# Performance work log

Hardware: AMD Instinct MI355X
Metric: run time of the kernel (lower is better)

## Reference

```python
import jax, jax.numpy as jnp
from jax import lax
import numpy as np

I, H, O = 4, 64, 4  # input_size, hidden_size, fc out


def setup_inputs() -> dict:
    key = jax.random.key(0)
    ks = jax.random.split(key, 7)
    B, T = 2048, 512
    s_ih = 1.0 / np.sqrt(H)  # PyTorch default init scale
    x = jax.random.normal(ks[0], (B, T, I), dtype=jnp.float32)
    W_ih = jax.random.uniform(ks[1], (4 * H, I), minval=-s_ih, maxval=s_ih, dtype=jnp.float32)
    W_hh = jax.random.uniform(ks[2], (4 * H, H), minval=-s_ih, maxval=s_ih, dtype=jnp.float32)
    b_ih = jax.random.uniform(ks[3], (4 * H,), minval=-s_ih, maxval=s_ih, dtype=jnp.float32)
    b_hh = jax.random.uniform(ks[4], (4 * H,), minval=-s_ih, maxval=s_ih, dtype=jnp.float32)
    W_fc = jax.random.uniform(ks[5], (O, H), minval=-s_ih, maxval=s_ih, dtype=jnp.float32)
    b_fc = jax.random.uniform(ks[6], (O,), minval=-s_ih, maxval=s_ih, dtype=jnp.float32)
    return {"x": x, "W_ih": W_ih, "W_hh": W_hh, "b_ih": b_ih, "b_hh": b_hh,
            "W_fc": W_fc, "b_fc": b_fc}


def reference(x, W_ih, W_hh, b_ih, b_hh, W_fc, b_fc):
    B = x.shape[0]
    # Precompute input contribution to all gates for every timestep: [B, T, 4H]
    xg = jnp.einsum('bti,gi->btg', x, W_ih) + (b_ih + b_hh)

    def step(carry, xt):
        h, c = carry                      # [B, H], [B, H]
        gates = xt + h @ W_hh.T           # [B, 4H]; PyTorch gate order i,f,g,o
        i, f, g, o = jnp.split(gates, 4, axis=-1)
        c = jax.nn.sigmoid(f) * c + jax.nn.sigmoid(i) * jnp.tanh(g)
        h = jax.nn.sigmoid(o) * jnp.tanh(c)
        return (h, c), None

    h0 = jnp.zeros((B, H), dtype=x.dtype)
    (h, c), _ = lax.scan(step, (h0, h0), jnp.swapaxes(xg, 0, 1))  # scan over T
    hidden = h[None]                      # [1, B, H] (num_layers*dirs = 1)
    return hidden @ W_fc.T + b_fc         # [1, B, O]
```

## Files before the change

kernel.cpp:

```cpp
#include <hip/hip_runtime.h>

typedef _Float16 half8 __attribute__((ext_vector_type(8)));
typedef _Float16 half4 __attribute__((ext_vector_type(4)));
typedef float f32x4 __attribute__((ext_vector_type(4)));

#define TT 512
#define HH 64
#define MB 8
#define S  72
#define XS 2056

__device__ __forceinline__ float xor8(float v) {
    return __builtin_bit_cast(float,
        __builtin_amdgcn_update_dpp(0, __builtin_bit_cast(int, v),
                                    0x128 ,
                                    0xF, 0xF, true));
}

__global__ __launch_bounds__(512, 1)
void lstm_v12(const float* __restrict__ x,
              const float* __restrict__ W_ih,
              const float* __restrict__ W_hh,
              const float* __restrict__ b_ih,
              const float* __restrict__ b_hh,
              const float* __restrict__ W_fc,
              const float* __restrict__ b_fc,
              float* __restrict__ out)
{
    __shared__ __align__(16) _Float16 st[2][8 * S];
    __shared__ __align__(16) _Float16 xbuf[MB * XS];

    const int tid = threadIdx.x;
    const int w   = tid >> 6;
    const int l   = tid & 63;
    const int q   = l >> 4;
    const int col = l & 15;
    const int b0  = blockIdx.x * MB;
    const int xcol = col & 7;
    const bool lo = (col < 8);

    const float kN = -1.4426950408889634f;
    const float kP =  2.8853900817779268f;

    half8 aw[2][3];
    #pragma unroll
    for (int p = 0; p < 2; ++p) {
        const int r = 64 * (col & 3) + 8 * w + 2 * (col >> 2) + p;
        const float scale = ((col & 3) == 2) ? kP : kN;
        #pragma unroll
        for (int c = 0; c < 2; ++c) {
            const float* src = W_hh + r * HH + 32 * c + 8 * q;
            half8 v;
            #pragma unroll
            for (int j = 0; j < 8; ++j) v[j] = (_Float16)(src[j] * scale);
            aw[p][c] = v;
        }
        half8 v = {};
        if (q == 0) {
            #pragma unroll
            for (int j = 0; j < 4; ++j) v[j] = (_Float16)(W_ih[r * 4 + j] * scale);
            v[4] = (_Float16)((b_ih[r] + b_hh[r]) * scale);
        }
        aw[p][2] = v;
    }

    #pragma unroll
    for (int it = 0; it < (MB * TT) / 512; ++it) {
        const int task = tid + it * 512;
        const int b = task >> 9, t = task & 511;
        float4 v = *(const float4*)(x + ((size_t)(b0 + b) * TT + t) * 4);
        half4 hx;
        hx[0] = (_Float16)v.x; hx[1] = (_Float16)v.y;
        hx[2] = (_Float16)v.z; hx[3] = (_Float16)v.w;
        *(half4*)&xbuf[b * XS + t * 4] = hx;
    }

    {
        _Float16* p0 = &st[0][0];
        for (int i = tid; i < 2 * 8 * S; i += 512) p0[i] = (_Float16)0.f;
    }
    __syncthreads();

    float cs = 0.f;
    const int wrow = xcol * S + 8 * w + 2 * q + (col >> 3);
    const _Float16 hone = (_Float16)1.0f, hzer = (_Float16)0.f;
    const f32x4 z4 = {0.f, 0.f, 0.f, 0.f};

    f32x4 accx0, accx1;
    {
        half4 xv = *(const half4*)&xbuf[xcol * XS + 0];
        half8 bx = {xv[0], xv[1], xv[2], xv[3], hone, hzer, hzer, hzer};
        accx0 = __builtin_amdgcn_mfma_f32_16x16x32_f16(aw[0][2], bx, z4, 0, 0, 0);
        accx1 = __builtin_amdgcn_mfma_f32_16x16x32_f16(aw[1][2], bx, z4, 0, 0, 0);
    }

    #pragma unroll 4
    for (int t = 0; t < TT; ++t) {
        const int rb = t & 1, wb = rb ^ 1;
        const _Float16* sr = &st[rb][0];

        half8 bh0 = *(const half8*)&sr[xcol * S +      8 * q];
        half8 bh1 = *(const half8*)&sr[xcol * S + 32 + 8 * q];
        half4 xv2 = *(const half4*)&xbuf[xcol * XS + (t + 1) * 4];

        f32x4 a0 = __builtin_amdgcn_mfma_f32_16x16x32_f16(aw[0][0], bh0, accx0, 0, 0, 0);
        f32x4 a1 = __builtin_amdgcn_mfma_f32_16x16x32_f16(aw[1][0], bh0, accx1, 0, 0, 0);
        a0 = __builtin_amdgcn_mfma_f32_16x16x32_f16(aw[0][1], bh1, a0, 0, 0, 0);
        a1 = __builtin_amdgcn_mfma_f32_16x16x32_f16(aw[1][1], bh1, a1, 0, 0, 0);

        {
            half8 bx2 = {xv2[0], xv2[1], xv2[2], xv2[3], hone, hzer, hzer, hzer};
            accx0 = __builtin_amdgcn_mfma_f32_16x16x32_f16(aw[0][2], bx2, z4, 0, 0, 0);
            accx1 = __builtin_amdgcn_mfma_f32_16x16x32_f16(aw[1][2], bx2, z4, 0, 0, 0);
        }

        const float s0 = xor8(a1[0]);
        const float s1 = xor8(a1[1]);
        const float s2 = xor8(a1[2]);
        const float s3 = xor8(a1[3]);
        const float gi = lo ? a0[0] : s0;
        const float gf = lo ? a0[1] : s1;
        const float gg = lo ? a0[2] : s2;
        const float go = lo ? a0[3] : s3;

        const float EI = __builtin_amdgcn_exp2f(gi);
        const float EF = __builtin_amdgcn_exp2f(gf);
        const float EG = __builtin_amdgcn_exp2f(gg);
        const float rF = __builtin_amdgcn_rcpf(1.f + EF);
        const float r1 = __builtin_amdgcn_rcpf((1.f + EI) * (EG + 1.f));
        cs = cs * rF + (EG - 1.f) * r1;
        const float EO = __builtin_amdgcn_exp2f(go);
        const float EC = __builtin_amdgcn_exp2f(kP * cs);
        const float r2 = __builtin_amdgcn_rcpf((1.f + EO) * (EC + 1.f));
        const float hn = (EC - 1.f) * r2;

        st[wb][wrow] = (_Float16)hn;
        __syncthreads();
    }

    if (tid < MB * 4) {
        const int b = tid >> 2, o = tid & 3;
        float s = b_fc[o];
        const float* wf = W_fc + o * HH;
        #pragma unroll
        for (int k = 0; k < HH; ++k)
            s = fmaf((float)st[0][b * S + k], wf[k], s);
        out[(size_t)(b0 + b) * 4 + o] = s;
    }
}

extern "C" void kernel_launch(void* const* d_in, const int* in_sizes, int n_in,
                              void* d_out, int out_size, void* d_ws, size_t ws_size,
                              hipStream_t stream) {
    const float* x    = (const float*)d_in[0];
    const float* W_ih = (const float*)d_in[1];
    const float* W_hh = (const float*)d_in[2];
    const float* b_ih = (const float*)d_in[3];
    const float* b_hh = (const float*)d_in[4];
    const float* W_fc = (const float*)d_in[5];
    const float* b_fc = (const float*)d_in[6];
    float* out = (float*)d_out;
    lstm_v12<<<2048 / MB, 512, 0, stream>>>(x, W_ih, W_hh, b_ih, b_hh, W_fc, b_fc, out);
}
```

Measured before the change: 229.0 us.

## Shrink LSTM blocks to 4 batch rows with 4 waves and 2 blocks per CU

Each block now handles 4 batch sequences with 256 threads (4 waves), and each wave computes 16 hidden units through 4 MFMA tiles instead of 2. This removes the DPP cross-lane shuffle, since each lane picks its gate values from the right tile with selects. Launch bounds now allow 2 blocks per CU and the grid doubles to 512 blocks. The aim is cheaper per-step barriers across fewer waves and more blocks to overlap each other's serial time steps. In exchange each wave issues twice the MFMAs per step, and 3 of every 4 tile columns are wasted because only 4 batch columns are live.

```diff
diff --git a/kernel.cpp b/kernel.cpp
--- a/kernel.cpp
+++ b/kernel.cpp
@@ -6,19 +6,12 @@
 
 #define TT 512
 #define HH 64
-#define MB 8
-#define S  72
+#define MB 4
+#define S  88
 #define XS 2056
 
-__device__ __forceinline__ float xor8(float v) {
-    return __builtin_bit_cast(float,
-        __builtin_amdgcn_update_dpp(0, __builtin_bit_cast(int, v),
-                                    0x128 ,
-                                    0xF, 0xF, true));
-}
-
-__global__ __launch_bounds__(512, 1)
-void lstm_v12(const float* __restrict__ x,
+__global__ __launch_bounds__(256, 2)
+void lstm_v13(const float* __restrict__ x,
               const float* __restrict__ W_ih,
               const float* __restrict__ W_hh,
               const float* __restrict__ b_ih,
@@ -27,7 +20,7 @@
               const float* __restrict__ b_fc,
               float* __restrict__ out)
 {
-    __shared__ __align__(16) _Float16 st[2][8 * S];
+    __shared__ __align__(16) _Float16 st[2][MB * S];
     __shared__ __align__(16) _Float16 xbuf[MB * XS];
 
     const int tid = threadIdx.x;
@@ -35,17 +28,17 @@
     const int l   = tid & 63;
     const int q   = l >> 4;
     const int col = l & 15;
+    const int bt  = col & 3;
+    const int g   = col >> 2;
     const int b0  = blockIdx.x * MB;
-    const int xcol = col & 7;
-    const bool lo = (col < 8);
 
     const float kN = -1.4426950408889634f;
     const float kP =  2.8853900817779268f;
 
-    half8 aw[2][3];
+    half8 aw[4][3];
     #pragma unroll
-    for (int p = 0; p < 2; ++p) {
-        const int r = 64 * (col & 3) + 8 * w + 2 * (col >> 2) + p;
+    for (int p = 0; p < 4; ++p) {
+        const int r = 64 * (col & 3) + 16 * w + 4 * p + (col >> 2);
         const float scale = ((col & 3) == 2) ? kP : kN;
         #pragma unroll
         for (int c = 0; c < 2; ++c) {
@@ -65,8 +58,8 @@
     }
 
     #pragma unroll
-    for (int it = 0; it < (MB * TT) / 512; ++it) {
-        const int task = tid + it * 512;
+    for (int it = 0; it < (MB * TT) / 256; ++it) {
+        const int task = tid + it * 256;
         const int b = task >> 9, t = task & 511;
         float4 v = *(const float4*)(x + ((size_t)(b0 + b) * TT + t) * 4);
         half4 hx;
@@ -75,23 +68,23 @@
         *(half4*)&xbuf[b * XS + t * 4] = hx;
     }
 
-    {
-        _Float16* p0 = &st[0][0];
-        for (int i = tid; i < 2 * 8 * S; i += 512) p0[i] = (_Float16)0.f;
-    }
+    for (int i = tid; i < 2 * MB * S; i += 256) (&st[0][0])[i] = (_Float16)0.f;
     __syncthreads();
 
     float cs = 0.f;
-    const int wrow = xcol * S + 8 * w + 2 * q + (col >> 3);
+    const int wrow = bt * S + 16 * w + 4 * g + q;
     const _Float16 hone = (_Float16)1.0f, hzer = (_Float16)0.f;
     const f32x4 z4 = {0.f, 0.f, 0.f, 0.f};
+    const bool s1 = (g & 1) != 0, s2 = (g & 2) != 0;
 
-    f32x4 accx0, accx1;
+    f32x4 accx0, accx1, accx2, accx3;
     {
-        half4 xv = *(const half4*)&xbuf[xcol * XS + 0];
+        half4 xv = *(const half4*)&xbuf[bt * XS + 0];
         half8 bx = {xv[0], xv[1], xv[2], xv[3], hone, hzer, hzer, hzer};
         accx0 = __builtin_amdgcn_mfma_f32_16x16x32_f16(aw[0][2], bx, z4, 0, 0, 0);
         accx1 = __builtin_amdgcn_mfma_f32_16x16x32_f16(aw[1][2], bx, z4, 0, 0, 0);
+        accx2 = __builtin_amdgcn_mfma_f32_16x16x32_f16(aw[2][2], bx, z4, 0, 0, 0);
+        accx3 = __builtin_amdgcn_mfma_f32_16x16x32_f16(aw[3][2], bx, z4, 0, 0, 0);
     }
 
     #pragma unroll 4
@@ -99,29 +92,33 @@
         const int rb = t & 1, wb = rb ^ 1;
         const _Float16* sr = &st[rb][0];
 
-        half8 bh0 = *(const half8*)&sr[xcol * S +      8 * q];
-        half8 bh1 = *(const half8*)&sr[xcol * S + 32 + 8 * q];
-        half4 xv2 = *(const half4*)&xbuf[xcol * XS + (t + 1) * 4];
+        half8 bh0 = *(const half8*)&sr[bt * S +      8 * q];
+        half8 bh1 = *(const half8*)&sr[bt * S + 32 + 8 * q];
+        half4 xv2 = *(const half4*)&xbuf[bt * XS + (t + 1) * 4];
 
         f32x4 a0 = __builtin_amdgcn_mfma_f32_16x16x32_f16(aw[0][0], bh0, accx0, 0, 0, 0);
         f32x4 a1 = __builtin_amdgcn_mfma_f32_16x16x32_f16(aw[1][0], bh0, accx1, 0, 0, 0);
+        f32x4 a2 = __builtin_amdgcn_mfma_f32_16x16x32_f16(aw[2][0], bh0, accx2, 0, 0, 0);
+        f32x4 a3 = __builtin_amdgcn_mfma_f32_16x16x32_f16(aw[3][0], bh0, accx3, 0, 0, 0);
         a0 = __builtin_amdgcn_mfma_f32_16x16x32_f16(aw[0][1], bh1, a0, 0, 0, 0);
         a1 = __builtin_amdgcn_mfma_f32_16x16x32_f16(aw[1][1], bh1, a1, 0, 0, 0);
+        a2 = __builtin_amdgcn_mfma_f32_16x16x32_f16(aw[2][1], bh1, a2, 0, 0, 0);
+        a3 = __builtin_amdgcn_mfma_f32_16x16x32_f16(aw[3][1], bh1, a3, 0, 0, 0);
 
         {
             half8 bx2 = {xv2[0], xv2[1], xv2[2], xv2[3], hone, hzer, hzer, hzer};
             accx0 = __builtin_amdgcn_mfma_f32_16x16x32_f16(aw[0][2], bx2, z4, 0, 0, 0);
             accx1 = __builtin_amdgcn_mfma_f32_16x16x32_f16(aw[1][2], bx2, z4, 0, 0, 0);
+            accx2 = __builtin_amdgcn_mfma_f32_16x16x32_f16(aw[2][2], bx2, z4, 0, 0, 0);
+            accx3 = __builtin_amdgcn_mfma_f32_16x16x32_f16(aw[3][2], bx2, z4, 0, 0, 0);
         }
 
-        const float s0 = xor8(a1[0]);
-        const float s1 = xor8(a1[1]);
-        const float s2 = xor8(a1[2]);
-        const float s3 = xor8(a1[3]);
-        const float gi = lo ? a0[0] : s0;
-        const float gf = lo ? a0[1] : s1;
-        const float gg = lo ? a0[2] : s2;
-        const float go = lo ? a0[3] : s3;
+        #define SEL(j) (s2 ? (s1 ? a3[j] : a2[j]) : (s1 ? a1[j] : a0[j]))
+        const float gi = SEL(0);
+        const float gf = SEL(1);
+        const float gg = SEL(2);
+        const float go = SEL(3);
+        #undef SEL
 
         const float EI = __builtin_amdgcn_exp2f(gi);
         const float EF = __builtin_amdgcn_exp2f(gf);
@@ -160,5 +157,5 @@
     const float* W_fc = (const float*)d_in[5];
     const float* b_fc = (const float*)d_in[6];
     float* out = (float*)d_out;
-    lstm_v12<<<2048 / MB, 512, 0, stream>>>(x, W_ih, W_hh, b_ih, b_hh, W_fc, b_fc, out);
+    lstm_v13<<<2048 / MB, 256, 0, stream>>>(x, W_ih, W_hh, b_ih, b_hh, W_fc, b_fc, out);
 }
```

Measured after the change: 247.8 us. 1.08x slower.

## Prefetch input MFMA one step ahead and store pre-padded x in LDS

Applied to the files above, without the earlier changes.

The x buffer in LDS now stores each timestep as a half8 with the bias-one and zero padding already in place, so the recurrent loop loads the MFMA operand directly without rebuilding a vector. The input-projection MFMAs for the next step are issued before the recurrent MFMAs, and the x load runs two steps ahead, to move that work off the critical h-dependent chain. The cell state is kept pre-scaled by the tanh exponent constant, which removes one multiply from the serial c-to-h path. It also changes LDS padding strides, and xbuf now takes about twice as much LDS.

```diff
diff --git a/kernel.cpp b/kernel.cpp
--- a/kernel.cpp
+++ b/kernel.cpp
@@ -7,8 +7,8 @@
 #define TT 512
 #define HH 64
 #define MB 8
-#define S  72
-#define XS 2056
+#define S  88
+#define XS 4112
 
 __device__ __forceinline__ float xor8(float v) {
     return __builtin_bit_cast(float,
@@ -18,7 +18,7 @@
 }
 
 __global__ __launch_bounds__(512, 1)
-void lstm_v12(const float* __restrict__ x,
+void lstm_v17(const float* __restrict__ x,
               const float* __restrict__ W_ih,
               const float* __restrict__ W_hh,
               const float* __restrict__ b_ih,
@@ -69,29 +69,28 @@
         const int task = tid + it * 512;
         const int b = task >> 9, t = task & 511;
         float4 v = *(const float4*)(x + ((size_t)(b0 + b) * TT + t) * 4);
-        half4 hx;
+        half8 hx;
         hx[0] = (_Float16)v.x; hx[1] = (_Float16)v.y;
         hx[2] = (_Float16)v.z; hx[3] = (_Float16)v.w;
-        *(half4*)&xbuf[b * XS + t * 4] = hx;
+        hx[4] = (_Float16)1.0f; hx[5] = (_Float16)0.f;
+        hx[6] = (_Float16)0.f;  hx[7] = (_Float16)0.f;
+        *(half8*)&xbuf[b * XS + t * 8] = hx;
     }
 
-    {
-        _Float16* p0 = &st[0][0];
-        for (int i = tid; i < 2 * 8 * S; i += 512) p0[i] = (_Float16)0.f;
-    }
+    for (int i = tid; i < 2 * 8 * S; i += 512) (&st[0][0])[i] = (_Float16)0.f;
     __syncthreads();
 
-    float cs = 0.f;
+    float cs2 = 0.f;
     const int wrow = xcol * S + 8 * w + 2 * q + (col >> 3);
-    const _Float16 hone = (_Float16)1.0f, hzer = (_Float16)0.f;
     const f32x4 z4 = {0.f, 0.f, 0.f, 0.f};
 
     f32x4 accx0, accx1;
+    half8 bxn;
     {
-        half4 xv = *(const half4*)&xbuf[xcol * XS + 0];
-        half8 bx = {xv[0], xv[1], xv[2], xv[3], hone, hzer, hzer, hzer};
-        accx0 = __builtin_amdgcn_mfma_f32_16x16x32_f16(aw[0][2], bx, z4, 0, 0, 0);
-        accx1 = __builtin_amdgcn_mfma_f32_16x16x32_f16(aw[1][2], bx, z4, 0, 0, 0);
+        half8 bx0 = *(const half8*)&xbuf[xcol * XS + 0];
+        accx0 = __builtin_amdgcn_mfma_f32_16x16x32_f16(aw[0][2], bx0, z4, 0, 0, 0);
+        accx1 = __builtin_amdgcn_mfma_f32_16x16x32_f16(aw[1][2], bx0, z4, 0, 0, 0);
+        bxn = *(const half8*)&xbuf[xcol * XS + 8];
     }
 
     #pragma unroll 4
@@ -101,18 +100,16 @@
 
         half8 bh0 = *(const half8*)&sr[xcol * S +      8 * q];
         half8 bh1 = *(const half8*)&sr[xcol * S + 32 + 8 * q];
-        half4 xv2 = *(const half4*)&xbuf[xcol * XS + (t + 1) * 4];
+
+        f32x4 axn0 = __builtin_amdgcn_mfma_f32_16x16x32_f16(aw[0][2], bxn, z4, 0, 0, 0);
+        f32x4 axn1 = __builtin_amdgcn_mfma_f32_16x16x32_f16(aw[1][2], bxn, z4, 0, 0, 0);
+
+        bxn = *(const half8*)&xbuf[xcol * XS + (t + 2) * 8];
 
         f32x4 a0 = __builtin_amdgcn_mfma_f32_16x16x32_f16(aw[0][0], bh0, accx0, 0, 0, 0);
         f32x4 a1 = __builtin_amdgcn_mfma_f32_16x16x32_f16(aw[1][0], bh0, accx1, 0, 0, 0);
         a0 = __builtin_amdgcn_mfma_f32_16x16x32_f16(aw[0][1], bh1, a0, 0, 0, 0);
         a1 = __builtin_amdgcn_mfma_f32_16x16x32_f16(aw[1][1], bh1, a1, 0, 0, 0);
-
-        {
-            half8 bx2 = {xv2[0], xv2[1], xv2[2], xv2[3], hone, hzer, hzer, hzer};
-            accx0 = __builtin_amdgcn_mfma_f32_16x16x32_f16(aw[0][2], bx2, z4, 0, 0, 0);
-            accx1 = __builtin_amdgcn_mfma_f32_16x16x32_f16(aw[1][2], bx2, z4, 0, 0, 0);
-        }
 
         const float s0 = xor8(a1[0]);
         const float s1 = xor8(a1[1]);
@@ -128,14 +125,17 @@
         const float EG = __builtin_amdgcn_exp2f(gg);
         const float rF = __builtin_amdgcn_rcpf(1.f + EF);
         const float r1 = __builtin_amdgcn_rcpf((1.f + EI) * (EG + 1.f));
-        cs = cs * rF + (EG - 1.f) * r1;
+        const float Y  = (kP * (EG - 1.f)) * r1;
+        cs2 = cs2 * rF + Y;
         const float EO = __builtin_amdgcn_exp2f(go);
-        const float EC = __builtin_amdgcn_exp2f(kP * cs);
+        const float EC = __builtin_amdgcn_exp2f(cs2);
         const float r2 = __builtin_amdgcn_rcpf((1.f + EO) * (EC + 1.f));
         const float hn = (EC - 1.f) * r2;
 
         st[wb][wrow] = (_Float16)hn;
         __syncthreads();
+
+        accx0 = axn0; accx1 = axn1;
     }
 
     if (tid < MB * 4) {
@@ -160,5 +160,5 @@
     const float* W_fc = (const float*)d_in[5];
     const float* b_fc = (const float*)d_in[6];
     float* out = (float*)d_out;
-    lstm_v12<<<2048 / MB, 512, 0, stream>>>(x, W_ih, W_hh, b_ih, b_hh, W_fc, b_fc, out);
+    lstm_v17<<<2048 / MB, 512, 0, stream>>>(x, W_ih, W_hh, b_ih, b_hh, W_fc, b_fc, out);
 }
```

Result: faster. 212.7 us (-7.2%).
